# Kernel tuning notes

Hardware: AMD Instinct MI355X
Metric: run time of the kernel (lower is better)

Reference implementation:

```python
import jax, jax.numpy as jnp
import numpy as np

B = 256   # number of segments
P = 2000  # points per segment (hard-coded by fc_1 = Linear(2000*32, 1024))
C = 32    # point feature channels
EPS_BN = 1e-5


def _bn_relu(h, g, b):
    # BatchNorm1d in training mode: batch statistics over axis 0, biased variance.
    m = jnp.mean(h, axis=0)
    v = jnp.var(h, axis=0)
    return jax.nn.relu((h - m) * jax.lax.rsqrt(v + EPS_BN) * g + b)


def setup_inputs() -> dict:
    key = jax.random.key(0)
    ks = jax.random.split(key, 16)
    s = 0.02
    inp = {
        "x": jax.random.normal(ks[0], (B * P, C), jnp.float32),
        "length": jnp.full((B,), P, dtype=jnp.int32),
        # attention MLP (1x1 conv1d chain 32->16->8->1), torch layout [out,in]
        "w1": jax.random.normal(ks[1], (16, 32), jnp.float32) * s,
        "b1": jnp.zeros((16,), jnp.float32),
        "g1": jnp.ones((16,), jnp.float32),
        "be1": jnp.zeros((16,), jnp.float32),
        "w2": jax.random.normal(ks[2], (8, 16), jnp.float32) * s,
        "b2": jnp.zeros((8,), jnp.float32),
        "g2": jnp.ones((8,), jnp.float32),
        "be2": jnp.zeros((8,), jnp.float32),
        "w3": jax.random.normal(ks[3], (1, 8), jnp.float32) * s,
        "b3": jnp.zeros((1,), jnp.float32),
        "g3": jnp.ones((1,), jnp.float32),
        "be3": jnp.zeros((1,), jnp.float32),
        # FC head
        "fw1": jax.random.normal(ks[4], (1024, P * C), jnp.float32) * s,
        "fb1": jnp.zeros((1024,), jnp.float32),
        "fg1": jnp.ones((1024,), jnp.float32),
        "fbe1": jnp.zeros((1024,), jnp.float32),
        "fw2": jax.random.normal(ks[5], (256, 1024), jnp.float32) * s,
        "fb2": jnp.zeros((256,), jnp.float32),
        "fg2": jnp.ones((256,), jnp.float32),
        "fbe2": jnp.zeros((256,), jnp.float32),
    }
    return inp


def reference(x, length, w1, b1, g1, be1, w2, b2, g2, be2, w3, b3, g3, be3,
              fw1, fb1, fg1, fbe1, fw2, fb2, fg2, fbe2):
    # Pointwise attention score MLP over all points (BN stats over the full
    # point dimension, matching conv1d+BatchNorm1d with batch size 1).
    h = _bn_relu(x @ w1.T + b1, g1, be1)          # [N,16]
    h = _bn_relu(h @ w2.T + b2, g2, be2)          # [N,8]
    score = _bn_relu(h @ w3.T + b3, g3, be3)      # [N,1]

    # Per-segment softmax over the point dim, then weighted features + flatten.
    # All segments have exactly P=2000 points (required by fc_1's input dim),
    # so the ragged slicing collapses to a dense [B,P,*] reshape.
    att = jax.nn.softmax(score.reshape(B, P, 1), axis=1)   # [B,P,1]
    pooled = (x.reshape(B, P, C) * att).reshape(B, P * C)  # [B,64000]

    r = _bn_relu(pooled @ fw1.T + fb1, fg1, fbe1)  # [B,1024]
    r = _bn_relu(r @ fw2.T + fb2, fg2, fbe2)       # [B,256]

    # F.normalize(p=2, dim=1, eps=1e-12)
    norm = jnp.maximum(jnp.linalg.norm(r, axis=1, keepdims=True), 1e-12)
    return r / norm
```

## Files before the change

kernel.cpp:

```cpp
#include <hip/hip_runtime.h>
#include <hip/hip_bf16.h>

#define NPTS   512000
#define PSEG   2000
#define INV_N  (1.0f/512000.0f)
#define EPS_BN 1e-5f

#define S1_OFF 0
#define S2_OFF 1024
#define S3_OFF 1536
#define S4_OFF 1600
#define S5_OFF 9792

using u32 = unsigned int;
using u16 = unsigned short;
using f32x4  = __attribute__((ext_vector_type(4))) float;
using bf16x8 = __attribute__((ext_vector_type(8))) short;

static __device__ __forceinline__ u16 f2bf(float f) {
    u32 u = __builtin_bit_cast(u32, f);
    u += 0x7fffu + ((u >> 16) & 1u);
    return (u16)(u >> 16);
}

static __device__ __forceinline__ void gload_lds16(const void* g, void* l) {
    __builtin_amdgcn_global_load_lds(
        (const __attribute__((address_space(1))) unsigned int*)g,
        (__attribute__((address_space(3))) unsigned int*)l, 16, 0, 0);
}

__global__ __launch_bounds__(256) void k_zero(float4* __restrict__ p) {
    p[blockIdx.x * 256 + threadIdx.x] = float4{0.0f, 0.0f, 0.0f, 0.0f};
}

__global__ __launch_bounds__(256) void k_mlp1(const float* __restrict__ x,
                                              const float* __restrict__ w1,
                                              float* __restrict__ a1,
                                              float* __restrict__ stats) {
    __shared__ float w[512];
    __shared__ float part[4][32];
    const int t = threadIdx.x;
    w[t] = w1[t]; w[t + 256] = w1[t + 256];
    __syncthreads();

    const int idx = blockIdx.x * 256 + t;
    const float4* xr = (const float4*)(x + (size_t)idx * 32);
    float4 xv[8];
#pragma unroll
    for (int i = 0; i < 8; i++) xv[i] = xr[i];

    float h[16];
#pragma unroll
    for (int c = 0; c < 16; c++) {
        float s = 0.0f;
        const float4* wr = (const float4*)(w + c * 32);
#pragma unroll
        for (int i = 0; i < 8; i++) {
            float4 wv = wr[i];
            s += xv[i].x * wv.x + xv[i].y * wv.y + xv[i].z * wv.z + xv[i].w * wv.w;
        }
        h[c] = s;
    }

    float4* ar = (float4*)(a1 + (size_t)idx * 16);
#pragma unroll
    for (int i = 0; i < 4; i++) {
        float4 o; o.x = h[i*4+0]; o.y = h[i*4+1]; o.z = h[i*4+2]; o.w = h[i*4+3];
        ar[i] = o;
    }

    const int lane = t & 63, wave = t >> 6;
#pragma unroll
    for (int c = 0; c < 16; c++) {
        float s = h[c], q = h[c] * h[c];
#pragma unroll
        for (int off = 32; off > 0; off >>= 1) {
            s += __shfl_down(s, off);
            q += __shfl_down(q, off);
        }
        if (lane == 0) { part[wave][c] = s; part[wave][16 + c] = q; }
    }
    __syncthreads();
    if (t < 32) {
        float tot = part[0][t] + part[1][t] + part[2][t] + part[3][t];
        atomicAdd(&stats[S1_OFF + (blockIdx.x & 31) * 32 + t], tot);
    }
}

__global__ __launch_bounds__(256) void k_mlp2(const float* __restrict__ a1,
                                              const float* __restrict__ w2,
                                              const float* __restrict__ g1,
                                              const float* __restrict__ be1,
                                              float* __restrict__ a2,
                                              float* __restrict__ stats) {
    __shared__ float w[128];
    __shared__ float sc[16], sh[16];
    __shared__ float part[4][16];
    const int t = threadIdx.x;
    if (t < 128) w[t] = w2[t];
    if (t < 16) {
        float s = 0.0f, q = 0.0f;
#pragma unroll 8
        for (int c = 0; c < 32; c++) {
            s += stats[S1_OFF + c * 32 + t];
            q += stats[S1_OFF + c * 32 + 16 + t];
        }
        float m = s * INV_N;
        float v = q * INV_N - m * m;
        float sl = g1[t] * rsqrtf(v + EPS_BN);
        sc[t] = sl; sh[t] = be1[t] - m * sl;
    }
    __syncthreads();

    const int idx = blockIdx.x * 256 + t;
    const float4* ar = (const float4*)(a1 + (size_t)idx * 16);
    float h[16];
#pragma unroll
    for (int i = 0; i < 4; i++) {
        float4 v4 = ar[i];
        h[i*4+0] = v4.x; h[i*4+1] = v4.y; h[i*4+2] = v4.z; h[i*4+3] = v4.w;
    }
#pragma unroll
    for (int c = 0; c < 16; c++) h[c] = fmaxf(fmaf(h[c], sc[c], sh[c]), 0.0f);

    float o[8];
#pragma unroll
    for (int c = 0; c < 8; c++) {
        float s = 0.0f;
#pragma unroll
        for (int k = 0; k < 16; k++) s += h[k] * w[c * 16 + k];
        o[c] = s;
    }
    float4* orp = (float4*)(a2 + (size_t)idx * 8);
    float4 o0; o0.x=o[0]; o0.y=o[1]; o0.z=o[2]; o0.w=o[3];
    float4 o1; o1.x=o[4]; o1.y=o[5]; o1.z=o[6]; o1.w=o[7];
    orp[0] = o0; orp[1] = o1;

    const int lane = t & 63, wave = t >> 6;
#pragma unroll
    for (int c = 0; c < 8; c++) {
        float s = o[c], q = o[c] * o[c];
#pragma unroll
        for (int off = 32; off > 0; off >>= 1) {
            s += __shfl_down(s, off);
            q += __shfl_down(q, off);
        }
        if (lane == 0) { part[wave][c] = s; part[wave][8 + c] = q; }
    }
    __syncthreads();
    if (t < 16) {
        float tot = part[0][t] + part[1][t] + part[2][t] + part[3][t];
        atomicAdd(&stats[S2_OFF + (blockIdx.x & 31) * 16 + t], tot);
    }
}

__global__ __launch_bounds__(256) void k_mlp3(const float* __restrict__ a2,
                                              const float* __restrict__ w3,
                                              const float* __restrict__ g2,
                                              const float* __restrict__ be2,
                                              float* __restrict__ a3,
                                              float* __restrict__ stats) {
    __shared__ float w[8], sc[8], sh[8];
    __shared__ float part[4][2];
    const int t = threadIdx.x;
    if (t < 8) {
        w[t] = w3[t];
        float s = 0.0f, q = 0.0f;
#pragma unroll 8
        for (int c = 0; c < 32; c++) {
            s += stats[S2_OFF + c * 16 + t];
            q += stats[S2_OFF + c * 16 + 8 + t];
        }
        float m = s * INV_N;
        float v = q * INV_N - m * m;
        float sl = g2[t] * rsqrtf(v + EPS_BN);
        sc[t] = sl; sh[t] = be2[t] - m * sl;
    }
    __syncthreads();

    const int idx = blockIdx.x * 256 + t;
    const float4* ar = (const float4*)(a2 + (size_t)idx * 8);
    float4 v0 = ar[0], v1 = ar[1];
    float h[8] = {v0.x, v0.y, v0.z, v0.w, v1.x, v1.y, v1.z, v1.w};
    float s = 0.0f;
#pragma unroll
    for (int c = 0; c < 8; c++) s += fmaxf(fmaf(h[c], sc[c], sh[c]), 0.0f) * w[c];
    a3[idx] = s;

    const int lane = t & 63, wave = t >> 6;
    float q = s * s;
    float ss = s;
#pragma unroll
    for (int off = 32; off > 0; off >>= 1) {
        ss += __shfl_down(ss, off);
        q  += __shfl_down(q, off);
    }
    if (lane == 0) { part[wave][0] = ss; part[wave][1] = q; }
    __syncthreads();
    if (t < 2) {
        float tot = part[0][t] + part[1][t] + part[2][t] + part[3][t];
        atomicAdd(&stats[S3_OFF + (blockIdx.x & 31) * 2 + t], tot);
    }
}

__global__ __launch_bounds__(256) void k_pool(const float* __restrict__ a3,
                                              const float* __restrict__ x,
                                              const float* __restrict__ g3,
                                              const float* __restrict__ be3,
                                              const float* __restrict__ stats,
                                              u16* __restrict__ pooled) {
    const int b = blockIdx.x, t = threadIdx.x;
    float sm = 0.0f, sq = 0.0f;
#pragma unroll 8
    for (int c = 0; c < 32; c++) {
        sm += stats[S3_OFF + c * 2];
        sq += stats[S3_OFF + c * 2 + 1];
    }
    const float m  = sm * INV_N;
    const float v  = sq * INV_N - m * m;
    const float sc = g3[0] * rsqrtf(v + EPS_BN);
    const float sh = be3[0] - m * sc;

    float sv[8];
    float mx = -1e30f;
#pragma unroll
    for (int i = 0; i < 8; i++) {
        int p = t + i * 256;
        if (p < PSEG) {
            float val = fmaxf(fmaf(a3[(size_t)b * PSEG + p], sc, sh), 0.0f);
            sv[i] = val; mx = fmaxf(mx, val);
        } else sv[i] = -1e30f;
    }
    const int lane = t & 63, wave = t >> 6;
    __shared__ float redm[4], reds[4];
#pragma unroll
    for (int off = 32; off > 0; off >>= 1) mx = fmaxf(mx, __shfl_xor(mx, off));
    if (lane == 0) redm[wave] = mx;
    __syncthreads();
    mx = fmaxf(fmaxf(redm[0], redm[1]), fmaxf(redm[2], redm[3]));

    float es = 0.0f;
#pragma unroll
    for (int i = 0; i < 8; i++) {
        int p = t + i * 256;
        if (p < PSEG) { float e = __expf(sv[i] - mx); sv[i] = e; es += e; }
    }
#pragma unroll
    for (int off = 32; off > 0; off >>= 1) es += __shfl_xor(es, off);
    if (lane == 0) reds[wave] = es;
    __syncthreads();
    const float inv = 1.0f / (reds[0] + reds[1] + reds[2] + reds[3]);

    const int swz = (b & 7) << 3;
#pragma unroll
    for (int i = 0; i < 8; i++) {
        int p = t + i * 256;
        if (p >= PSEG) continue;
        const float att = sv[i] * inv;
        const float4* xr = (const float4*)(x + ((size_t)b * PSEG + p) * 32);
        u16* dst = pooled + (size_t)b * 64000 + (size_t)(p >> 1) * 64;
        const int half = (p & 1) << 5;
#pragma unroll
        for (int u = 0; u < 4; u++) {
            float4 f0 = xr[u * 2], f1 = xr[u * 2 + 1];
            u32 q0 = (u32)f2bf(f0.x * att) | ((u32)f2bf(f0.y * att) << 16);
            u32 q1 = (u32)f2bf(f0.z * att) | ((u32)f2bf(f0.w * att) << 16);
            u32 q2 = (u32)f2bf(f1.x * att) | ((u32)f2bf(f1.y * att) << 16);
            u32 q3 = (u32)f2bf(f1.z * att) | ((u32)f2bf(f1.w * att) << 16);
            uint4 q; q.x = q0; q.y = q1; q.z = q2; q.w = q3;
            *(uint4*)(dst + ((half | (u << 3)) ^ swz)) = q;
        }
    }
}

__global__ __launch_bounds__(256) void k_gemm4(const u16* __restrict__ pooled,
                                               const float* __restrict__ fw1,
                                               float* __restrict__ a4p) {
    __shared__ alignas(16) char smem[81920];

    const int t = threadIdx.x;
    const int jblk = blockIdx.x;
    const int kblk = blockIdx.y;
    const int wave = t >> 6, lane = t & 63;
    const int kbase = kblk * 1600;

    const u16* gA = pooled + (size_t)(wave * 8 + (lane >> 3)) * 64000 + (lane & 7) * 8;
    const int jj = t >> 4;
    const int ks = (t & 15) * 4;

    f32x4 acc[4][4] = {};
    float4 bn0, bn1, bn2, bn3;

    {
#pragma unroll
        for (int i = 0; i < 8; i++)
            gload_lds16(gA + kbase + (size_t)i * 32 * 64000,
                        smem + wave * 1024 + i * 4096);
        const float* bsrc = fw1 + (size_t)(jblk * 64 + jj) * 64000 + kbase + ks;
        bn0 = *(const float4*)(bsrc);
        bn1 = *(const float4*)(bsrc + (size_t)16 * 64000);
        bn2 = *(const float4*)(bsrc + (size_t)32 * 64000);
        bn3 = *(const float4*)(bsrc + (size_t)48 * 64000);
        char* Bs = smem + 32768;
#pragma unroll
        for (int i = 0; i < 4; i++) {
            const int j = i * 16 + jj;
            float4 v = (i == 0) ? bn0 : (i == 1) ? bn1 : (i == 2) ? bn2 : bn3;
            ushort4 bv;
            bv.x = f2bf(v.x); bv.y = f2bf(v.y); bv.z = f2bf(v.z); bv.w = f2bf(v.w);
            *(ushort4*)(Bs + ((j * 128 + ks * 2) ^ ((j & 7) << 4))) = bv;
        }
    }
    __syncthreads();

    int curoff = 0;
    for (int step = 0; step < 25; ++step) {
        const int nxtoff = curoff ^ 40960;
        const bool pf = (step + 1 < 25);
        if (pf) {
            const int k1 = kbase + (step + 1) * 64;
            const float* bsrc = fw1 + (size_t)(jblk * 64 + jj) * 64000 + k1 + ks;
            bn0 = *(const float4*)(bsrc);
            bn1 = *(const float4*)(bsrc + (size_t)16 * 64000);
            bn2 = *(const float4*)(bsrc + (size_t)32 * 64000);
            bn3 = *(const float4*)(bsrc + (size_t)48 * 64000);
#pragma unroll
            for (int i = 0; i < 8; i++)
                gload_lds16(gA + k1 + (size_t)i * 32 * 64000,
                            smem + nxtoff + wave * 1024 + i * 4096);
        }
        const char* As = smem + curoff;
        const char* Bs = smem + curoff + 32768;
#pragma unroll
        for (int kk = 0; kk < 2; ++kk) {
            const int krow = kk * 32 + (lane >> 4) * 8;
            bf16x8 aF[4], bF[4];
#pragma unroll
            for (int mm = 0; mm < 4; mm++) {
                const int row = wave * 64 + mm * 16 + (lane & 15);
                aF[mm] = *(const bf16x8*)(As + ((row * 128 + krow * 2) ^ ((row & 7) << 4)));
            }
#pragma unroll
            for (int nn = 0; nn < 4; nn++) {
                const int col = nn * 16 + (lane & 15);
                bF[nn] = *(const bf16x8*)(Bs + ((col * 128 + krow * 2) ^ ((col & 7) << 4)));
            }
#pragma unroll
            for (int mm = 0; mm < 4; mm++)
#pragma unroll
                for (int nn = 0; nn < 4; nn++)
                    acc[mm][nn] = __builtin_amdgcn_mfma_f32_16x16x32_bf16(
                        aF[mm], bF[nn], acc[mm][nn], 0, 0, 0);
        }
        if (pf) {
            char* Bn = smem + nxtoff + 32768;
#pragma unroll
            for (int i = 0; i < 4; i++) {
                const int j = i * 16 + jj;
                float4 v = (i == 0) ? bn0 : (i == 1) ? bn1 : (i == 2) ? bn2 : bn3;
                ushort4 bv;
                bv.x = f2bf(v.x); bv.y = f2bf(v.y); bv.z = f2bf(v.z); bv.w = f2bf(v.w);
                *(ushort4*)(Bn + ((j * 128 + ks * 2) ^ ((j & 7) << 4))) = bv;
            }
        }
        __syncthreads();
        curoff = nxtoff;
    }

    float* dst = a4p + (size_t)kblk * 262144;
#pragma unroll
    for (int mm = 0; mm < 4; mm++)
#pragma unroll
        for (int nn = 0; nn < 4; nn++)
#pragma unroll
            for (int r = 0; r < 4; r++) {
                const int row = wave * 64 + mm * 16 + (lane >> 4) * 4 + r;
                const int col = jblk * 64 + nn * 16 + (lane & 15);
                dst[(size_t)row * 1024 + col] = acc[mm][nn][r];
            }
}

__global__ __launch_bounds__(256) void k_red4(const float* __restrict__ a4p,
                                              float* __restrict__ a4,
                                              float* __restrict__ stats) {
    const int i = blockIdx.x, t = threadIdx.x;
    float4 s = {0.0f, 0.0f, 0.0f, 0.0f};
#pragma unroll 8
    for (int kb = 0; kb < 40; kb++) {
        float4 v = *(const float4*)(a4p + (size_t)kb * 262144 + (size_t)i * 1024 + t * 4);
        s.x += v.x; s.y += v.y; s.z += v.z; s.w += v.w;
    }
    *(float4*)(a4 + (size_t)i * 1024 + t * 4) = s;
    const int j = t * 4;
    float* s4 = stats + S4_OFF + (i & 3) * 2048;
    atomicAdd(&s4[j + 0], s.x);
    atomicAdd(&s4[j + 1], s.y);
    atomicAdd(&s4[j + 2], s.z);
    atomicAdd(&s4[j + 3], s.w);
    atomicAdd(&s4[1024 + j + 0], s.x * s.x);
    atomicAdd(&s4[1024 + j + 1], s.y * s.y);
    atomicAdd(&s4[1024 + j + 2], s.z * s.z);
    atomicAdd(&s4[1024 + j + 3], s.w * s.w);
}

__global__ __launch_bounds__(256) void k_fc2(const float* __restrict__ a4,
                                             const float* __restrict__ fg1,
                                             const float* __restrict__ fbe1,
                                             const float* __restrict__ fw2,
                                             float* __restrict__ stats,
                                             float* __restrict__ a5) {
    __shared__ alignas(16) float h[1024];
    const int i = blockIdx.x, t = threadIdx.x;
#pragma unroll
    for (int u = 0; u < 4; u++) {
        const int k = u * 256 + t;
        float s = 0.0f, q = 0.0f;
#pragma unroll
        for (int c = 0; c < 4; c++) {
            s += stats[S4_OFF + c * 2048 + k];
            q += stats[S4_OFF + c * 2048 + 1024 + k];
        }
        float m  = s * (1.0f / 256.0f);
        float v  = q * (1.0f / 256.0f) - m * m;
        float sc = fg1[k] * rsqrtf(v + EPS_BN);
        float sh = fbe1[k] - m * sc;
        h[k] = fmaxf(fmaf(a4[(size_t)i * 1024 + k], sc, sh), 0.0f);
    }
    __syncthreads();
    const float4* wr = (const float4*)(fw2 + (size_t)t * 1024);
    const float4* hr = (const float4*)h;
    float s = 0.0f;
#pragma unroll 4
    for (int u = 0; u < 256; u++) {
        float4 w = wr[u], hv = hr[u];
        s += w.x * hv.x + w.y * hv.y + w.z * hv.z + w.w * hv.w;
    }
    a5[(size_t)i * 256 + t] = s;
    float* s5 = stats + S5_OFF + (i & 15) * 512;
    atomicAdd(&s5[t], s);
    atomicAdd(&s5[256 + t], s * s);
}

__global__ __launch_bounds__(256) void k_norm(const float* __restrict__ a5,
                                              const float* __restrict__ fg2,
                                              const float* __restrict__ fbe2,
                                              const float* __restrict__ stats,
                                              float* __restrict__ out) {
    const int i = blockIdx.x, t = threadIdx.x;
    float s = 0.0f, q2 = 0.0f;
#pragma unroll
    for (int c = 0; c < 16; c++) {
        s  += stats[S5_OFF + c * 512 + t];
        q2 += stats[S5_OFF + c * 512 + 256 + t];
    }
    float m  = s * (1.0f / 256.0f);
    float v  = q2 * (1.0f / 256.0f) - m * m;
    float sc = fg2[t] * rsqrtf(v + EPS_BN);
    float sh = fbe2[t] - m * sc;
    float r = fmaxf(fmaf(a5[(size_t)i * 256 + t], sc, sh), 0.0f);

    float q = r * r;
    const int lane = t & 63, wave = t >> 6;
#pragma unroll
    for (int off = 32; off > 0; off >>= 1) q += __shfl_xor(q, off);
    __shared__ float red[4];
    if (lane == 0) red[wave] = q;
    __syncthreads();
    float tot = red[0] + red[1] + red[2] + red[3];
    float nrm = fmaxf(sqrtf(tot), 1e-12f);
    out[(size_t)i * 256 + t] = r / nrm;
}

extern "C" void kernel_launch(void* const* d_in, const int* in_sizes, int n_in,
                              void* d_out, int out_size, void* d_ws, size_t ws_size,
                              hipStream_t stream) {
    const float* x   = (const float*)d_in[0];
    const float* w1  = (const float*)d_in[2];
    const float* g1  = (const float*)d_in[4];
    const float* be1 = (const float*)d_in[5];
    const float* w2  = (const float*)d_in[6];
    const float* g2  = (const float*)d_in[8];
    const float* be2 = (const float*)d_in[9];
    const float* w3  = (const float*)d_in[10];
    const float* g3  = (const float*)d_in[12];
    const float* be3 = (const float*)d_in[13];
    const float* fw1 = (const float*)d_in[14];
    const float* fg1 = (const float*)d_in[16];
    const float* fbe1= (const float*)d_in[17];
    const float* fw2 = (const float*)d_in[18];
    const float* fg2 = (const float*)d_in[20];
    const float* fbe2= (const float*)d_in[21];
    float* out = (float*)d_out;

    char* ws = (char*)d_ws;
    float* stats = (float*)ws;
    float* a4 = (float*)(ws + 73728);
    float* a5 = (float*)(ws + 73728 + 1048576);
    float* a4p = (float*)(ws + 73728 + 1048576 + 262144);
    char*  big = ws + 73728 + 1048576 + 262144 + 41943040;
    float* a1 = (float*)big;
    u16*   pooled = (u16*)big;
    float* a2 = (float*)(big + 32768000);
    float* a3 = (float*)(big + 32768000 + 16384000);

    k_zero<<<18, 256, 0, stream>>>((float4*)ws);
    k_mlp1<<<2000, 256, 0, stream>>>(x, w1, a1, stats);
    k_mlp2<<<2000, 256, 0, stream>>>(a1, w2, g1, be1, a2, stats);
    k_mlp3<<<2000, 256, 0, stream>>>(a2, w3, g2, be2, a3, stats);
    k_pool<<<256, 256, 0, stream>>>(a3, x, g3, be3, stats, pooled);
    k_gemm4<<<dim3(16, 40), 256, 0, stream>>>(pooled, fw1, a4p);
    k_red4<<<256, 256, 0, stream>>>(a4p, a4, stats);
    k_fc2<<<256, 256, 0, stream>>>(a4, fg1, fbe1, fw2, stats, a5);
    k_norm<<<256, 256, 0, stream>>>(a5, fg2, fbe2, stats, out);
}
```

Measured before the change: 274.0 us.

## Single-buffer A tile in LDS for gemm4 to cut shared memory footprint

Shrinks k_gemm4 LDS from 80KB to 48KB by keeping A in one buffer and double-buffering only the converted B tile. The A global-to-LDS loads are now issued after a barrier that ends the MFMA phase, and are waited on immediately, with explicit sched_barriers and s_barriers in place of __syncthreads. The aim is to fit more blocks per CU for better occupancy, at the cost of no longer overlapping the A tile load with compute.

```diff
diff --git a/kernel.cpp b/kernel.cpp
--- a/kernel.cpp
+++ b/kernel.cpp
@@ -276,7 +276,7 @@
 __global__ __launch_bounds__(256) void k_gemm4(const u16* __restrict__ pooled,
                                                const float* __restrict__ fw1,
                                                float* __restrict__ a4p) {
-    __shared__ alignas(16) char smem[81920];
+    __shared__ alignas(16) char smem[49152];
 
     const int t = threadIdx.x;
     const int jblk = blockIdx.x;
@@ -287,50 +287,48 @@
     const u16* gA = pooled + (size_t)(wave * 8 + (lane >> 3)) * 64000 + (lane & 7) * 8;
     const int jj = t >> 4;
     const int ks = (t & 15) * 4;
+    const float* gB = fw1 + (size_t)(jblk * 64 + jj) * 64000 + ks;
 
     f32x4 acc[4][4] = {};
-    float4 bn0, bn1, bn2, bn3;
-
+    float4 b0, b1, b2, b3;
+
+#pragma unroll
+    for (int i = 0; i < 8; i++)
+        gload_lds16(gA + kbase + (size_t)i * 32 * 64000,
+                    smem + wave * 1024 + i * 4096);
     {
-#pragma unroll
-        for (int i = 0; i < 8; i++)
-            gload_lds16(gA + kbase + (size_t)i * 32 * 64000,
-                        smem + wave * 1024 + i * 4096);
-        const float* bsrc = fw1 + (size_t)(jblk * 64 + jj) * 64000 + kbase + ks;
-        bn0 = *(const float4*)(bsrc);
-        bn1 = *(const float4*)(bsrc + (size_t)16 * 64000);
-        bn2 = *(const float4*)(bsrc + (size_t)32 * 64000);
-        bn3 = *(const float4*)(bsrc + (size_t)48 * 64000);
+        const float* bs = gB + kbase;
+        b0 = *(const float4*)(bs);
+        b1 = *(const float4*)(bs + (size_t)16 * 64000);
+        b2 = *(const float4*)(bs + (size_t)32 * 64000);
+        b3 = *(const float4*)(bs + (size_t)48 * 64000);
         char* Bs = smem + 32768;
 #pragma unroll
         for (int i = 0; i < 4; i++) {
             const int j = i * 16 + jj;
-            float4 v = (i == 0) ? bn0 : (i == 1) ? bn1 : (i == 2) ? bn2 : bn3;
+            float4 v = (i == 0) ? b0 : (i == 1) ? b1 : (i == 2) ? b2 : b3;
             ushort4 bv;
             bv.x = f2bf(v.x); bv.y = f2bf(v.y); bv.z = f2bf(v.z); bv.w = f2bf(v.w);
             *(ushort4*)(Bs + ((j * 128 + ks * 2) ^ ((j & 7) << 4))) = bv;
         }
     }
-    __syncthreads();
-
-    int curoff = 0;
+    asm volatile("s_waitcnt vmcnt(0) lgkmcnt(0)" ::: "memory");
+    __builtin_amdgcn_s_barrier();
+    __builtin_amdgcn_sched_barrier(0);
+
+    int cur = 0;
     for (int step = 0; step < 25; ++step) {
-        const int nxtoff = curoff ^ 40960;
         const bool pf = (step + 1 < 25);
         if (pf) {
-            const int k1 = kbase + (step + 1) * 64;
-            const float* bsrc = fw1 + (size_t)(jblk * 64 + jj) * 64000 + k1 + ks;
-            bn0 = *(const float4*)(bsrc);
-            bn1 = *(const float4*)(bsrc + (size_t)16 * 64000);
-            bn2 = *(const float4*)(bsrc + (size_t)32 * 64000);
-            bn3 = *(const float4*)(bsrc + (size_t)48 * 64000);
-#pragma unroll
-            for (int i = 0; i < 8; i++)
-                gload_lds16(gA + k1 + (size_t)i * 32 * 64000,
-                            smem + nxtoff + wave * 1024 + i * 4096);
-        }
-        const char* As = smem + curoff;
-        const char* Bs = smem + curoff + 32768;
+            const float* bs = gB + kbase + (step + 1) * 64;
+            b0 = *(const float4*)(bs);
+            b1 = *(const float4*)(bs + (size_t)16 * 64000);
+            b2 = *(const float4*)(bs + (size_t)32 * 64000);
+            b3 = *(const float4*)(bs + (size_t)48 * 64000);
+        }
+        __builtin_amdgcn_sched_barrier(0);
+        const char* As = smem;
+        const char* Bs = smem + 32768 + cur * 8192;
 #pragma unroll
         for (int kk = 0; kk < 2; ++kk) {
             const int krow = kk * 32 + (lane >> 4) * 8;
@@ -352,19 +350,30 @@
                     acc[mm][nn] = __builtin_amdgcn_mfma_f32_16x16x32_bf16(
                         aF[mm], bF[nn], acc[mm][nn], 0, 0, 0);
         }
+        __builtin_amdgcn_sched_barrier(0);
+        __builtin_amdgcn_s_barrier();
+        __builtin_amdgcn_sched_barrier(0);
         if (pf) {
-            char* Bn = smem + nxtoff + 32768;
+#pragma unroll
+            for (int i = 0; i < 8; i++)
+                gload_lds16(gA + kbase + (step + 1) * 64 + (size_t)i * 32 * 64000,
+                            smem + wave * 1024 + i * 4096);
+            __builtin_amdgcn_sched_barrier(0);
+            char* Bn = smem + 32768 + (cur ^ 1) * 8192;
 #pragma unroll
             for (int i = 0; i < 4; i++) {
                 const int j = i * 16 + jj;
-                float4 v = (i == 0) ? bn0 : (i == 1) ? bn1 : (i == 2) ? bn2 : bn3;
+                float4 v = (i == 0) ? b0 : (i == 1) ? b1 : (i == 2) ? b2 : b3;
                 ushort4 bv;
                 bv.x = f2bf(v.x); bv.y = f2bf(v.y); bv.z = f2bf(v.z); bv.w = f2bf(v.w);
                 *(ushort4*)(Bn + ((j * 128 + ks * 2) ^ ((j & 7) << 4))) = bv;
             }
-        }
-        __syncthreads();
-        curoff = nxtoff;
+            __builtin_amdgcn_sched_barrier(0);
+            asm volatile("s_waitcnt vmcnt(0) lgkmcnt(0)" ::: "memory");
+            __builtin_amdgcn_s_barrier();
+            __builtin_amdgcn_sched_barrier(0);
+        }
+        cur ^= 1;
     }
 
     float* dst = a4p + (size_t)kblk * 262144;
```

New measurement: 267.9 us. -2.2%, faster.
